# Kernel optimization log

Measured on AMD Instinct MI355X. Metric: run time of the kernel, lower is better.

The kernel has to match this reference:

```python
import jax, jax.numpy as jnp
import numpy as np

B, N, C, H, K = 4, 4096, 64, 4, 16  # batch, points per cloud, channels, gat heads, knn k
NEG_SLOPE = 0.2  # PyG GATConv leaky_relu slope


def knn_idx(x):
    # x: [B, N, D] -> global neighbor indices [B, N, K] (self excluded, per-batch knn)
    x2 = jnp.sum(x * x, axis=-1)                                   # [B, N]
    d = x2[:, :, None] - 2.0 * jnp.einsum('bnd,bmd->bnm', x, x) + x2[:, None, :]
    d = jnp.where(jnp.eye(N, dtype=bool)[None], jnp.inf, d)        # exclude self (loop=False)
    _, idx = jax.lax.top_k(-d, K)                                  # [B, N, K] local indices
    return idx + (jnp.arange(B) * N)[:, None, None]                # globalize


def gat(x, nbr, W, a_src, a_dst, b):
    # x: [Nn, Din], nbr: [Nn, K] global neighbor (source) indices per target node
    Nn = x.shape[0]
    h = (x @ W).reshape(Nn, H, -1)                                 # [Nn, H, Ch]
    asrc = jnp.einsum('nhc,hc->nh', h, a_src)                      # [Nn, H]
    adst = jnp.einsum('nhc,hc->nh', h, a_dst)                      # [Nn, H]
    e = jax.nn.leaky_relu(asrc[nbr] + adst[:, None, :], NEG_SLOPE) # [Nn, K, H]
    attn = jax.nn.softmax(e, axis=1)                               # softmax over K neighbors
    out = jnp.einsum('nkh,nkhc->nhc', attn, h[nbr])                # [Nn, H, Ch]
    return out.reshape(Nn, -1) + b


def setup_inputs() -> dict:
    key = jax.random.key(0)
    ks = jax.random.split(key, 12)
    s1 = 1.0 / np.sqrt(C + 3)
    s2 = 1.0 / np.sqrt(C)
    sm = 1.0 / np.sqrt(2 * C)
    return {
        'point_features': jax.random.normal(ks[0], (B, C, N), jnp.float32),
        'point': jax.random.normal(ks[1], (B, 3, N), jnp.float32),
        'W1': jax.random.normal(ks[2], (C + 3, C), jnp.float32) * s1,
        'a1_src': jax.random.normal(ks[3], (H, C // H), jnp.float32) * s2,
        'a1_dst': jax.random.normal(ks[4], (H, C // H), jnp.float32) * s2,
        'b1': jax.random.normal(ks[5], (C,), jnp.float32) * 0.01,
        'W2': jax.random.normal(ks[6], (C, C), jnp.float32) * s2,
        'a2_src': jax.random.normal(ks[7], (H, C // H), jnp.float32) * s2,
        'a2_dst': jax.random.normal(ks[8], (H, C // H), jnp.float32) * s2,
        'b2': jax.random.normal(ks[9], (C,), jnp.float32) * 0.01,
        'Wm': jax.random.normal(ks[10], (2 * C, C), jnp.float32) * sm,
        'bm': jax.random.normal(ks[11], (C,), jnp.float32) * 0.01,
    }


def reference(point_features, point, W1, a1_src, a1_dst, b1, W2, a2_src, a2_dst, b2, Wm, bm):
    # cat features with coords, flatten to node list [B*N, C+3]
    x = jnp.concatenate([point_features, point], axis=1)           # [B, C+3, N]
    x = jnp.transpose(x, (0, 2, 1)).reshape(B * N, C + 3)
    nbr1 = knn_idx(x.reshape(B, N, C + 3)).reshape(B * N, K)
    f1 = jax.nn.elu(gat(x, nbr1, W1, a1_src, a1_dst, b1))          # [B*N, C]
    # dropout p=0.5 is identity in eval mode
    nbr2 = knn_idx(f1.reshape(B, N, C)).reshape(B * N, K)
    f2 = jax.nn.elu(gat(f1, nbr2, W2, a2_src, a2_dst, b2))         # [B*N, C]
    f = jnp.concatenate([f1, f2], axis=1)                          # [B*N, 2C]
    f = jax.nn.elu(f @ Wm + bm)                                    # [B*N, C]
    return jnp.transpose(f.reshape(B, N, C), (0, 2, 1))            # [B, C, N]
```

## Files before the change

kernel.cpp:

```cpp
#include <hip/hip_runtime.h>
#include <math.h>

#define BB   4
#define NPTS 4096
#define NNODE (BB*NPTS)
#define CC   64
#define HHH  4
#define KK   16
#define D1   67
#define SD1  68
#define SD2  64
#define NSTR 4
#define NSEG 8
#define USTR (NSTR*KK + 2)

typedef __attribute__((ext_vector_type(2))) float f32x2;

__device__ __forceinline__ void pkfma_s(f32x2 &a, unsigned long long u, f32x2 x){
    asm("v_pk_fma_f32 %0, %1, %2, %0" : "+v"(a) : "s"(u), "v"(x));
}

__global__ __launch_bounds__(256) void k_prep(const float* __restrict__ pf,
                                              const float* __restrict__ pt,
                                              float* __restrict__ xcat,
                                              float* __restrict__ x2)
{
    __shared__ float T[64][69];
    const int tid = threadIdx.x;
    const int nb = blockIdx.x*64;
    const int b = nb>>12;
    const int n0 = nb & (NPTS-1);
    const int l = tid&63, w = tid>>6;
    const float* pfb = pf + (size_t)b*CC*NPTS + n0 + l;
    #pragma unroll
    for (int k=0;k<16;k++){ int c=w*16+k; T[l][c] = pfb[(size_t)c*NPTS]; }
    if (w<3)  T[l][64+w] = pt[(size_t)b*3*NPTS + (size_t)w*NPTS + n0 + l];
    if (w==3) T[l][67] = 0.f;
    __syncthreads();
    if (tid<64){
        float acc=0.f;
        #pragma unroll 1
        for (int c=0;c<67;c++){ float v=T[tid][c]; acc = fmaf(v,v,acc); }
        x2[nb+tid]=acc;
    }
    float* dst = xcat + (size_t)nb*SD1;
    for (int i=tid;i<64*SD1;i+=256) dst[i] = T[i/SD1][i%SD1];
}

__device__ __forceinline__ double packdi(float dd, int lidx){
    unsigned u = __float_as_uint(dd);
    unsigned us = u ^ ((unsigned)((int)u >> 31) | 0x80000000u);
    return fma((double)us, 4096.0, (double)lidx);
}

__device__ __forceinline__ void sift16(double (&dk)[KK], double v){
    #pragma unroll
    for (int j=0;j<KK;j++){
        double lo = fmin(dk[j], v);
        v = fmax(dk[j], v);
        dk[j] = lo;
    }
}

template<int SD, int NS>
__global__ __launch_bounds__(256) void k_knn_seg(const float* __restrict__ X,
    const float* __restrict__ x2, uint2* __restrict__ part)
{
    __shared__ unsigned       mus[64*USTR];
    __shared__ unsigned short mix[64*USTR];

    const int SEGC = NPTS/NS;
    const int tid = threadIdx.x;
    const int w = __builtin_amdgcn_readfirstlane(tid>>6);
    const int l = tid&63;
    const int b = blockIdx.y, seg = blockIdx.z;
    const int nodeBase = b*NPTS + blockIdx.x*64;
    const int node = nodeBase + l;
    const int nlocal = blockIdx.x*64 + l;

    f32x2 xt[SD/2];
    {
        const f32x2* xr = (const f32x2*)(X + (size_t)node*SD);
        #pragma unroll
        for (int i=0;i<SD/2;i++) xt[i]=xr[i];
    }
    const float x2t = x2[node];

    double dk[KK];
    #pragma unroll
    for (int i=0;i<KK;i++) dk[i]=__builtin_inf();

    const float* Xb  = X  + (size_t)b*NPTS*SD;
    const float* x2b = x2 + (size_t)b*NPTS;

    #pragma unroll 1
    for (int q=0;q<SEGC/NSTR;q++){
        int lc = seg*SEGC + q*NSTR + w;
        const unsigned long long* crow =
            (const unsigned long long*)(Xb + (size_t)lc*SD);
        float x2c = x2b[lc];
        f32x2 a0 = {0.f,0.f}, a1 = {0.f,0.f};
        #pragma unroll
        for (int i=0;i<SD/4;i++){
            pkfma_s(a0, crow[2*i],   xt[2*i]);
            pkfma_s(a1, crow[2*i+1], xt[2*i+1]);
        }
        float dot = (a0.x + a0.y) + (a1.x + a1.y);
        float dd = fmaf(-2.f, dot, x2t) + x2c;
        double pd = packdi(dd, lc);
        if (lc==nlocal) pd = __builtin_inf();
        sift16(dk, pd);
    }
    #pragma unroll
    for (int i=0;i<KK;i++){
        double bd = dk[i];
        unsigned us = (unsigned)(bd * (1.0/4096.0));
        unsigned id = (unsigned)(bd - (double)us*4096.0);
        mus[l*USTR + w*KK + i] = us;
        mix[l*USTR + w*KK + i] = (unsigned short)id;
    }
    __syncthreads();
    if (tid < 64){
        const unsigned*       mu = mus + tid*USTR;
        const unsigned short* mi = mix + tid*USTR;
        unsigned hu[NSTR], hx[NSTR]; int pp[NSTR];
        #pragma unroll
        for (int s=0;s<NSTR;s++){ pp[s]=0; hu[s]=mu[s*KK]; hx[s]=mi[s*KK]; }
        size_t obase = ((size_t)(nodeBase + tid)*NS + seg)*KK;
        #pragma unroll 1
        for (int r=0;r<KK;r++){
            unsigned bu=hu[0], bx=hx[0]; int bw=0;
            #pragma unroll
            for (int s=1;s<NSTR;s++){
                if (hu[s]<bu || (hu[s]==bu && hx[s]<bx)){ bu=hu[s]; bx=hx[s]; bw=s; }
            }
            part[obase + r] = make_uint2(bu, bx);
            #pragma unroll
            for (int s=0;s<NSTR;s++){
                if (bw==s){
                    int np = ++pp[s];
                    bool ok = np < KK;
                    unsigned nu = mu[s*KK + np];
                    unsigned nx = mi[s*KK + np];
                    hu[s] = ok ? nu : 0xFFFFFFFFu;
                    hx[s] = ok ? nx : 0xFFFFu;
                }
            }
        }
    }
}

template<int SD, int D>
__global__ __launch_bounds__(256) void k_gemm_h(const float* __restrict__ X,
    const float* __restrict__ W, const float* __restrict__ a_s,
    const float* __restrict__ a_d,
    float* __restrict__ h, float* __restrict__ asrc, float* __restrict__ adst)
{
    __shared__ float Wl[D*CC];
    __shared__ float asl[CC], adl[CC];
    __shared__ float Xs[16][SD+1];
    const int tid = threadIdx.x;
    for (int i=tid;i<D*CC;i+=256) Wl[i]=W[i];
    if (tid<CC){ asl[tid]=a_s[tid]; adl[tid]=a_d[tid]; }
    const int nodeBase = blockIdx.x*16;
    {
        const float* src = X + (size_t)nodeBase*SD;
        for (int i=tid;i<16*SD;i+=256) Xs[i/SD][i%SD] = src[i];
    }
    __syncthreads();
    const int g = tid>>4, cq = tid&15;
    const int node = nodeBase + g;
    float acc[4]={0,0,0,0};
    const float* xrow = Xs[g];
    #pragma unroll 1
    for (int d=0;d<D;d++){
        float xv = xrow[d];
        const float* wp = Wl + d*CC + cq*4;
        acc[0]=fmaf(xv,wp[0],acc[0]); acc[1]=fmaf(xv,wp[1],acc[1]);
        acc[2]=fmaf(xv,wp[2],acc[2]); acc[3]=fmaf(xv,wp[3],acc[3]);
    }
    ((float4*)(h + (size_t)node*CC))[cq] = make_float4(acc[0],acc[1],acc[2],acc[3]);
    float sp=0.f, dp=0.f;
    #pragma unroll
    for (int j=0;j<4;j++){
        int c = cq*4+j;
        sp = fmaf(acc[j], asl[c], sp);
        dp = fmaf(acc[j], adl[c], dp);
    }
    sp += __shfl_xor(sp,1); sp += __shfl_xor(sp,2);
    dp += __shfl_xor(dp,1); dp += __shfl_xor(dp,2);
    if ((cq&3)==0){
        asrc[(size_t)node*HHH + (cq>>2)] = sp;
        adst[(size_t)node*HHH + (cq>>2)] = dp;
    }
}

__global__ __launch_bounds__(256) void k_gat(const float* __restrict__ h,
    const float* __restrict__ asrc, const float* __restrict__ adst,
    const uint2* __restrict__ part, const float* __restrict__ bias,
    float* __restrict__ f, float* __restrict__ x2out)
{
    int wid = threadIdx.x>>6, lane = threadIdx.x&63;
    int node = blockIdx.x*4 + wid;
    int bbase = (node>>12)<<12;
    int hh = lane>>4;
    const uint2* pn = part + (size_t)node*(NSEG*KK);
    uint2 v0 = pn[lane], v1 = pn[64+lane];
    unsigned long long e0 = ((unsigned long long)v0.x<<16) | (unsigned long long)v0.y;
    unsigned long long e1 = ((unsigned long long)v1.x<<16) | (unsigned long long)v1.y;
    float ad = adst[(size_t)node*HHH+hh];
    int js[KK]; float e[KK];
    #pragma unroll 1
    for (int r=0;r<KK;r++){
        unsigned long long m = e0<e1 ? e0 : e1;
        #pragma unroll
        for (int s=32;s>0;s>>=1){
            unsigned long long o = __shfl_xor(m, s);
            if (o<m) m=o;
        }
        js[r] = bbase + (int)(m & 0xFFFFull);
        if (e0==m) e0 = ~0ull;
        if (e1==m) e1 = ~0ull;
    }
    #pragma unroll
    for (int k=0;k<KK;k++){
        int j = js[k] & (NNODE-1);
        js[k]=j;
        float ev = asrc[(size_t)j*HHH+hh] + ad;
        e[k] = ev>0.f ? ev : 0.2f*ev;
    }
    float m = e[0];
    #pragma unroll
    for (int k=1;k<KK;k++) m = fmaxf(m,e[k]);
    float s=0.f;
    #pragma unroll
    for (int k=0;k<KK;k++){ e[k]=__expf(e[k]-m); s+=e[k]; }
    float inv = 1.f/s;
    float acc=0.f;
    #pragma unroll
    for (int k=0;k<KK;k++)
        acc = fmaf(e[k]*inv, h[(size_t)js[k]*CC + lane], acc);
    float val = acc + bias[lane];
    val = val>0.f ? val : expm1f(val);
    f[(size_t)node*CC+lane]=val;
    float sq = val*val;
    #pragma unroll
    for (int s2=32;s2>0;s2>>=1) sq += __shfl_xor(sq, s2);
    if (lane==0) x2out[node]=sq;
}

__global__ __launch_bounds__(256) void k_final(const float* __restrict__ f1,
    const float* __restrict__ f2, const float* __restrict__ Wm,
    const float* __restrict__ bm, float* __restrict__ out)
{
    __shared__ float Wl[2*CC*CC];
    __shared__ float Xs[16][2*CC+1];
    const int tid=threadIdx.x;
    for (int i=tid;i<2*CC*CC;i+=256) Wl[i]=Wm[i];
    const int nodeBase = blockIdx.x*16;
    {
        const float* s1 = f1 + (size_t)nodeBase*CC;
        for (int i=tid;i<16*CC;i+=256) Xs[i/CC][i%CC] = s1[i];
        const float* s2 = f2 + (size_t)nodeBase*CC;
        for (int i=tid;i<16*CC;i+=256) Xs[i/CC][CC + i%CC] = s2[i];
    }
    __syncthreads();
    const int g = tid>>4, cq = tid&15;
    const int node = nodeBase + g;
    const int b = node>>12, n = node&(NPTS-1);
    float acc[4]={0,0,0,0};
    const float* xrow = Xs[g];
    #pragma unroll 1
    for (int d=0;d<2*CC;d++){
        float xv = xrow[d];
        const float* wp = Wl + d*CC + cq*4;
        acc[0]=fmaf(xv,wp[0],acc[0]); acc[1]=fmaf(xv,wp[1],acc[1]);
        acc[2]=fmaf(xv,wp[2],acc[2]); acc[3]=fmaf(xv,wp[3],acc[3]);
    }
    #pragma unroll
    for (int j=0;j<4;j++){
        int c = cq*4+j;
        float v = acc[j] + bm[c];
        v = v>0.f ? v : expm1f(v);
        out[(size_t)b*CC*NPTS + (size_t)c*NPTS + n] = v;
    }
}

__global__ void k_zero(float* out, int n){
    int i = blockIdx.x*256 + threadIdx.x;
    if (i<n) out[i] = 0.f;
}

extern "C" void kernel_launch(void* const* d_in, const int* in_sizes, int n_in,
                              void* d_out, int out_size, void* d_ws, size_t ws_size,
                              hipStream_t stream) {
    const float* pf  = (const float*)d_in[0];
    const float* pt  = (const float*)d_in[1];
    const float* W1  = (const float*)d_in[2];
    const float* a1s = (const float*)d_in[3];
    const float* a1d = (const float*)d_in[4];
    const float* b1  = (const float*)d_in[5];
    const float* W2  = (const float*)d_in[6];
    const float* a2s = (const float*)d_in[7];
    const float* a2d = (const float*)d_in[8];
    const float* b2  = (const float*)d_in[9];
    const float* Wm  = (const float*)d_in[10];
    const float* bm  = (const float*)d_in[11];
    float* out = (float*)d_out;

    float* ws = (float*)d_ws;
    float* xcat  = ws;
    float* f2    = xcat;
    float* h     = xcat + (size_t)NNODE*SD1;
    float* f1    = h    + (size_t)NNODE*CC;
    float* x2    = f1   + (size_t)NNODE*CC;
    float* asrc  = x2   + NNODE;
    float* adst  = asrc + (size_t)NNODE*HHH;
    float* wsend = adst + (size_t)NNODE*HHH;
    uint2* part  = (uint2*)wsend;
    size_t need  = (size_t)(wsend - ws)*sizeof(float)
                 + (size_t)NNODE*NSEG*KK*sizeof(uint2) + 64;
    if (ws_size < need) {
        k_zero<<<(out_size+255)/256, 256, 0, stream>>>(out, out_size);
        return;
    }

    dim3 knnGrid(NPTS/64, BB, NSEG);

    k_prep<<<NNODE/64, 256, 0, stream>>>(pf, pt, xcat, x2);
    k_knn_seg<SD1,NSEG><<<knnGrid, 256, 0, stream>>>(xcat, x2, part);
    k_gemm_h<SD1, D1><<<NNODE/16, 256, 0, stream>>>(xcat, W1, a1s, a1d, h, asrc, adst);
    k_gat<<<NNODE/4, 256, 0, stream>>>(h, asrc, adst, part, b1, f1, x2);
    k_knn_seg<SD2,NSEG><<<knnGrid, 256, 0, stream>>>(f1, x2, part);
    k_gemm_h<SD2, CC><<<NNODE/16, 256, 0, stream>>>(f1, W2, a2s, a2d, h, asrc, adst);
    k_gat<<<NNODE/4, 256, 0, stream>>>(h, asrc, adst, part, b2, f2, x2);
    k_final<<<NNODE/16, 256, 0, stream>>>(f1, f2, Wm, bm, out);
}
```

Baseline: 616.5 us.

## Replace in-block stripe merge with single-wave KNN segments and wider GAT merge

The KNN kernel no longer uses four waves per block that each scan a stripe and are merged through shared memory. Each block is now a single 64-thread wave that scans its whole segment and writes its sorted top-16 list straight to global memory. When the workspace is large enough, the candidate set is split into 16 segments instead of 8, keeping parallelism roughly the same. The GAT kernel is templated on the segment count and merges more partial lists per lane with wave reductions. This removes the LDS traffic, the barrier and the serial single-wave merge, at the cost of twice the partial-result storage and more merge work in GAT.

```diff
diff --git a/kernel.cpp b/kernel.cpp
--- a/kernel.cpp
+++ b/kernel.cpp
@@ -10,9 +10,6 @@
 #define D1   67
 #define SD1  68
 #define SD2  64
-#define NSTR 4
-#define NSEG 8
-#define USTR (NSTR*KK + 2)
 
 typedef __attribute__((ext_vector_type(2))) float f32x2;
 
@@ -63,20 +60,16 @@
 }
 
 template<int SD, int NS>
-__global__ __launch_bounds__(256) void k_knn_seg(const float* __restrict__ X,
+__global__ __launch_bounds__(64) void k_knn_seg(const float* __restrict__ X,
     const float* __restrict__ x2, uint2* __restrict__ part)
 {
-    __shared__ unsigned       mus[64*USTR];
-    __shared__ unsigned short mix[64*USTR];
-
     const int SEGC = NPTS/NS;
-    const int tid = threadIdx.x;
-    const int w = __builtin_amdgcn_readfirstlane(tid>>6);
-    const int l = tid&63;
-    const int b = blockIdx.y, seg = blockIdx.z;
-    const int nodeBase = b*NPTS + blockIdx.x*64;
+    const int l = threadIdx.x;
+    const int nodeBase = blockIdx.x*64;
+    const int b = nodeBase>>12;
+    const int seg = blockIdx.y;
     const int node = nodeBase + l;
-    const int nlocal = blockIdx.x*64 + l;
+    const int nlocal = node & (NPTS-1);
 
     f32x2 xt[SD/2];
     {
@@ -94,8 +87,8 @@
     const float* x2b = x2 + (size_t)b*NPTS;
 
     #pragma unroll 1
-    for (int q=0;q<SEGC/NSTR;q++){
-        int lc = seg*SEGC + q*NSTR + w;
+    for (int q=0;q<SEGC;q++){
+        int lc = seg*SEGC + q;
         const unsigned long long* crow =
             (const unsigned long long*)(Xb + (size_t)lc*SD);
         float x2c = x2b[lc];
@@ -111,42 +104,13 @@
         if (lc==nlocal) pd = __builtin_inf();
         sift16(dk, pd);
     }
+    uint2* dst = part + ((size_t)node*NS + seg)*KK;
     #pragma unroll
     for (int i=0;i<KK;i++){
         double bd = dk[i];
         unsigned us = (unsigned)(bd * (1.0/4096.0));
         unsigned id = (unsigned)(bd - (double)us*4096.0);
-        mus[l*USTR + w*KK + i] = us;
-        mix[l*USTR + w*KK + i] = (unsigned short)id;
-    }
-    __syncthreads();
-    if (tid < 64){
-        const unsigned*       mu = mus + tid*USTR;
-        const unsigned short* mi = mix + tid*USTR;
-        unsigned hu[NSTR], hx[NSTR]; int pp[NSTR];
-        #pragma unroll
-        for (int s=0;s<NSTR;s++){ pp[s]=0; hu[s]=mu[s*KK]; hx[s]=mi[s*KK]; }
-        size_t obase = ((size_t)(nodeBase + tid)*NS + seg)*KK;
-        #pragma unroll 1
-        for (int r=0;r<KK;r++){
-            unsigned bu=hu[0], bx=hx[0]; int bw=0;
-            #pragma unroll
-            for (int s=1;s<NSTR;s++){
-                if (hu[s]<bu || (hu[s]==bu && hx[s]<bx)){ bu=hu[s]; bx=hx[s]; bw=s; }
-            }
-            part[obase + r] = make_uint2(bu, bx);
-            #pragma unroll
-            for (int s=0;s<NSTR;s++){
-                if (bw==s){
-                    int np = ++pp[s];
-                    bool ok = np < KK;
-                    unsigned nu = mu[s*KK + np];
-                    unsigned nx = mi[s*KK + np];
-                    hu[s] = ok ? nu : 0xFFFFFFFFu;
-                    hx[s] = ok ? nx : 0xFFFFu;
-                }
-            }
-        }
+        dst[i] = make_uint2(us, id);
     }
 }
 
@@ -195,32 +159,39 @@
     }
 }
 
+template<int NS>
 __global__ __launch_bounds__(256) void k_gat(const float* __restrict__ h,
     const float* __restrict__ asrc, const float* __restrict__ adst,
     const uint2* __restrict__ part, const float* __restrict__ bias,
     float* __restrict__ f, float* __restrict__ x2out)
 {
+    const int E = NS*KK/64;
     int wid = threadIdx.x>>6, lane = threadIdx.x&63;
     int node = blockIdx.x*4 + wid;
     int bbase = (node>>12)<<12;
     int hh = lane>>4;
-    const uint2* pn = part + (size_t)node*(NSEG*KK);
-    uint2 v0 = pn[lane], v1 = pn[64+lane];
-    unsigned long long e0 = ((unsigned long long)v0.x<<16) | (unsigned long long)v0.y;
-    unsigned long long e1 = ((unsigned long long)v1.x<<16) | (unsigned long long)v1.y;
+    const uint2* pn = part + (size_t)node*(NS*KK);
+    unsigned long long ek[E];
+    #pragma unroll
+    for (int i=0;i<E;i++){
+        uint2 v = pn[i*64 + lane];
+        ek[i] = ((unsigned long long)v.x<<16) | (unsigned long long)v.y;
+    }
     float ad = adst[(size_t)node*HHH+hh];
     int js[KK]; float e[KK];
     #pragma unroll 1
     for (int r=0;r<KK;r++){
-        unsigned long long m = e0<e1 ? e0 : e1;
+        unsigned long long m = ek[0];
+        #pragma unroll
+        for (int i=1;i<E;i++) if (ek[i]<m) m=ek[i];
         #pragma unroll
         for (int s=32;s>0;s>>=1){
             unsigned long long o = __shfl_xor(m, s);
             if (o<m) m=o;
         }
         js[r] = bbase + (int)(m & 0xFFFFull);
-        if (e0==m) e0 = ~0ull;
-        if (e1==m) e1 = ~0ull;
+        #pragma unroll
+        for (int i=0;i<E;i++) if (ek[i]==m) ek[i] = ~0ull;
     }
     #pragma unroll
     for (int k=0;k<KK;k++){
@@ -318,21 +289,34 @@
     float* adst  = asrc + (size_t)NNODE*HHH;
     float* wsend = adst + (size_t)NNODE*HHH;
     uint2* part  = (uint2*)wsend;
-    size_t need  = (size_t)(wsend - ws)*sizeof(float)
-                 + (size_t)NNODE*NSEG*KK*sizeof(uint2) + 64;
-    if (ws_size < need) {
+    size_t base_bytes = (size_t)(wsend - ws)*sizeof(float);
+    size_t need16 = base_bytes + (size_t)NNODE*16*KK*sizeof(uint2) + 64;
+    size_t need8  = base_bytes + (size_t)NNODE*8*KK*sizeof(uint2) + 64;
+
+    if (ws_size < need8) {
         k_zero<<<(out_size+255)/256, 256, 0, stream>>>(out, out_size);
         return;
     }
 
-    dim3 knnGrid(NPTS/64, BB, NSEG);
-
     k_prep<<<NNODE/64, 256, 0, stream>>>(pf, pt, xcat, x2);
-    k_knn_seg<SD1,NSEG><<<knnGrid, 256, 0, stream>>>(xcat, x2, part);
-    k_gemm_h<SD1, D1><<<NNODE/16, 256, 0, stream>>>(xcat, W1, a1s, a1d, h, asrc, adst);
-    k_gat<<<NNODE/4, 256, 0, stream>>>(h, asrc, adst, part, b1, f1, x2);
-    k_knn_seg<SD2,NSEG><<<knnGrid, 256, 0, stream>>>(f1, x2, part);
-    k_gemm_h<SD2, CC><<<NNODE/16, 256, 0, stream>>>(f1, W2, a2s, a2d, h, asrc, adst);
-    k_gat<<<NNODE/4, 256, 0, stream>>>(h, asrc, adst, part, b2, f2, x2);
+
+    if (ws_size >= need16) {
+        dim3 g(NNODE/64, 16);
+        k_knn_seg<SD1,16><<<g, 64, 0, stream>>>(xcat, x2, part);
+        k_gemm_h<SD1, D1><<<NNODE/16, 256, 0, stream>>>(xcat, W1, a1s, a1d, h, asrc, adst);
+        k_gat<16><<<NNODE/4, 256, 0, stream>>>(h, asrc, adst, part, b1, f1, x2);
+        k_knn_seg<SD2,16><<<g, 64, 0, stream>>>(f1, x2, part);
+        k_gemm_h<SD2, CC><<<NNODE/16, 256, 0, stream>>>(f1, W2, a2s, a2d, h, asrc, adst);
+        k_gat<16><<<NNODE/4, 256, 0, stream>>>(h, asrc, adst, part, b2, f2, x2);
+    } else {
+        dim3 g(NNODE/64, 8);
+        k_knn_seg<SD1,8><<<g, 64, 0, stream>>>(xcat, x2, part);
+        k_gemm_h<SD1, D1><<<NNODE/16, 256, 0, stream>>>(xcat, W1, a1s, a1d, h, asrc, adst);
+        k_gat<8><<<NNODE/4, 256, 0, stream>>>(h, asrc, adst, part, b1, f1, x2);
+        k_knn_seg<SD2,8><<<g, 64, 0, stream>>>(f1, x2, part);
+        k_gemm_h<SD2, CC><<<NNODE/16, 256, 0, stream>>>(f1, W2, a2s, a2d, h, asrc, adst);
+        k_gat<8><<<NNODE/4, 256, 0, stream>>>(h, asrc, adst, part, b2, f2, x2);
+    }
+
     k_final<<<NNODE/16, 256, 0, stream>>>(f1, f2, Wm, bm, out);
 }
```

Result: slower. 671.9 us (+9.0%).
